# Performance work log

Hardware: AMD Instinct MI355X
Metric: run time of the kernel (lower is better)

## Reference

```python
import jax, jax.numpy as jnp
import numpy as np

BN_EPS = 1e-5


def _binary_activation(x):
    # forward value = sign(x); gradient flows through piecewise poly o3 (STE)
    s = jnp.sign(x)
    o1 = jnp.where(x < -1.0, -1.0, x * x + 2.0 * x)
    o2 = jnp.where(x < 0.0, o1, -x * x + 2.0 * x)
    o3 = jnp.where(x < 1.0, o2, 1.0)
    return jax.lax.stop_gradient(s - o3) + o3


def _binarize_weights(w):
    # sign_function: fwd 2*(w>0)-1, bwd identity (STE)
    sgn = 2.0 * (w > 0.0).astype(w.dtype) - 1.0
    wb = jax.lax.stop_gradient(sgn - w) + w
    # detached per-output-channel scale: mean |w| over (in, kh, kw)
    scale = jax.lax.stop_gradient(jnp.mean(jnp.abs(w), axis=(1, 2, 3), keepdims=True))
    return scale * wb


def setup_inputs() -> dict:
    key = jax.random.key(0)
    k1, k2, k3 = jax.random.split(key, 3)
    C = 64
    x = jax.random.normal(k1, (32, C, 112, 112), dtype=jnp.float32)
    w = jax.random.uniform(k2, (C, C, 3, 3), dtype=jnp.float32) * 0.001
    return {
        "x": x,
        "b0": jnp.zeros((1, C, 1, 1), jnp.float32),
        "w": w,
        "gamma": jnp.ones((C,), jnp.float32),
        "beta": jnp.zeros((C,), jnp.float32),
        "b1": jnp.zeros((1, C, 1, 1), jnp.float32),
        "alpha": jnp.full((C,), 0.25, jnp.float32),  # PReLU default init
        "b2": jnp.zeros((1, C, 1, 1), jnp.float32),
    }


def reference(x, b0, w, gamma, beta, b1, alpha, b2):
    residual = x
    out = x + b0                       # move0
    out = _binary_activation(out)      # binary activation
    bw = _binarize_weights(w)
    out = jax.lax.conv_general_dilated(
        out, bw, window_strides=(1, 1), padding=[(1, 1), (1, 1)],
        dimension_numbers=("NCHW", "OIHW", "NCHW"))
    # BatchNorm2d in training mode (batch stats, biased variance)
    mu = jnp.mean(out, axis=(0, 2, 3), keepdims=True)
    var = jnp.var(out, axis=(0, 2, 3), keepdims=True)
    g = gamma.reshape(1, -1, 1, 1)
    b = beta.reshape(1, -1, 1, 1)
    out = (out - mu) * jax.lax.rsqrt(var + BN_EPS) * g + b
    out = out + residual
    out = out + b1                     # move1
    a = alpha.reshape(1, -1, 1, 1)
    out = jnp.where(out > 0, out, a * out)  # PReLU
    out = out + b2                     # move2
    return out
```

## Files before the change

### kernel.cpp

```cpp
#include <hip/hip_runtime.h>
#include <stdint.h>

#define C 64
#define HH 112
#define WWD 112
#define HW (HH*WWD)
#define NB 32
#define MTOT (NB*HW)
#define PPR 56
#define PPI 6272
#define PACK_BLKS 1568
#define CONV_BLKS 25
#define OH 32

typedef unsigned long long u64t;

__global__ __launch_bounds__(256) void k_prep_pack(
        const float* __restrict__ x, const float* __restrict__ b0,
        const float* __restrict__ w,
        uint64_t* __restrict__ xp,
        uint64_t* __restrict__ wbits, float* __restrict__ wscale,
        int* __restrict__ corrP, int* __restrict__ ps, u64t* __restrict__ pq) {
    int bid = blockIdx.x;
    if (bid < PACK_BLKS) {
        int n = bid / 49;
        int pix = (bid % 49) * 256 + threadIdx.x;
        uint64_t p = 0;
        const float* xb = x + (size_t)n * C * HW + pix;
        #pragma unroll
        for (int c = 0; c < C; ++c) {
            float v = xb[(size_t)c * HW] + b0[c];
            p |= (uint64_t)(v > 0.f) << c;
        }
        xp[(size_t)n*HW + pix] = p;
    } else {
        int tid = threadIdx.x;
        int o = bid - PACK_BLKS;
        if (tid < 64) {
            int i = tid;
            const float* wp = w + ((size_t)o*C + i)*9;
            float s = 0.f;
            uint64_t b[9];
            #pragma unroll
            for (int k = 0; k < 9; ++k) {
                float v = wp[k];
                s += fabsf(v);
                b[k] = __ballot(v > 0.f);
            }
            #pragma unroll
            for (int off = 32; off > 0; off >>= 1) s += __shfl_down(s, off);
            if (i == 0) {
                wscale[o] = s * (1.0f/576.0f);
                int pq9[9];
                #pragma unroll
                for (int k = 0; k < 9; ++k) {
                    wbits[o*9+k] = b[k];
                    pq9[k] = __popcll(b[k]);
                }
                for (int rc = 0; rc < 3; ++rc)
                    for (int cc = 0; cc < 3; ++cc) {
                        int corr = 0;
                        for (int kr = 0; kr < 3; ++kr)
                            for (int kc = 0; kc < 3; ++kc) {
                                bool oob = (rc==0 && kr==0) || (rc==2 && kr==2) ||
                                           (cc==0 && kc==0) || (cc==2 && kc==2);
                                if (oob) corr += 64 - 2*pq9[kr*3+kc];
                            }
                        corrP[(rc*3+cc)*C + o] = 576 - corr;
                    }
            }
        } else if (bid == PACK_BLKS) {
            for (int i = tid - 64; i < C*8; i += 192) { ps[i] = 0; pq[i] = 0ull; }
        }
    }
}

__global__ __launch_bounds__(256) void k_convstats(
        const uint64_t* __restrict__ xp, const uint64_t* __restrict__ wbits,
        const int* __restrict__ corrP, int* __restrict__ ps, u64t* __restrict__ pq) {
    __shared__ uint64_t sq[OH*9];
    __shared__ int scor[9*OH];
    __shared__ int lsw[4][OH];
    __shared__ int lqw[4][OH];
    const int obase = blockIdx.z * OH;
    for (int i = threadIdx.x; i < OH*9; i += 256) sq[i] = wbits[obase*9 + i];
    for (int i = threadIdx.x; i < 9*OH; i += 256) {
        int r = i / OH, oo = i - r*OH;
        scor[i] = corrP[r*C + obase + oo];
    }
    __syncthreads();

    int n = blockIdx.y;
    int pr = blockIdx.x * 256 + threadIdx.x;
    int act = pr < PPI;
    int prc = act ? pr : (PPI - 1);
    int row = prc / PPR;
    int j   = prc - row * PPR;
    int c0  = 2 * j;
    const uint64_t* base = xp + (size_t)n * HW;
    uint64_t P[12];
    #pragma unroll
    for (int r = 0; r < 3; ++r) {
        int rr = row + r - 1;
        bool okr = (rr >= 0) & (rr < HH);
        #pragma unroll
        for (int c = 0; c < 4; ++c) {
            int cc = c0 + c - 1;
            bool ok = okr & (cc >= 0) & (cc < WWD);
            P[r*4+c] = ok ? base[(size_t)rr * WWD + cc] : 0ull;
        }
    }
    int rc   = (row == 0) ? 0 : ((row == HH-1) ? 2 : 1);
    int reg0 = (rc*3 + ((c0 == 0) ? 0 : 1)) * OH;
    int reg1 = (rc*3 + ((c0 == WWD-2) ? 2 : 1)) * OH;
    int wid = threadIdx.x >> 6, lane = threadIdx.x & 63;

    #pragma unroll 2
    for (int oo = 0; oo < OH; ++oo) {
        const uint64_t* q = &sq[oo*9];
        int a0 = 0, a1 = 0;
        #pragma unroll
        for (int r = 0; r < 3; ++r) {
            #pragma unroll
            for (int c = 0; c < 3; ++c) {
                uint64_t qk = q[r*3+c];
                a0 += __popcll(P[r*4+c]   ^ qk);
                a1 += __popcll(P[r*4+c+1] ^ qk);
            }
        }
        int v0 = scor[reg0 + oo] - 2*a0;
        int v1 = scor[reg1 + oo] - 2*a1;
        int s  = act ? (v0 + v1) : 0;
        int qq = act ? (v0*v0 + v1*v1) : 0;
        #pragma unroll
        for (int off = 1; off < 64; off <<= 1) {
            s  += __shfl_xor(s,  off);
            qq += __shfl_xor(qq, off);
        }
        if (lane == 0) { lsw[wid][oo] = s; lqw[wid][oo] = qq; }
    }
    __syncthreads();
    int t = threadIdx.x;
    int bkt = blockIdx.y & 7;
    if (t < OH) {
        int st = lsw[0][t] + lsw[1][t] + lsw[2][t] + lsw[3][t];
        atomicAdd(&ps[(obase + t)*8 + bkt], st);
    } else if (t < 2*OH) {
        int oo = t - OH;
        unsigned int qt = (unsigned)lqw[0][oo] + (unsigned)lqw[1][oo]
                        + (unsigned)lqw[2][oo] + (unsigned)lqw[3][oo];
        atomicAdd(&pq[(obase + oo)*8 + bkt], (u64t)qt);
    }
}

__global__ __launch_bounds__(256) void k_finish(
        const uint64_t* __restrict__ xp, const uint64_t* __restrict__ wbits,
        const int* __restrict__ corrP, const int* __restrict__ ps,
        const u64t* __restrict__ pq, const float* __restrict__ x,
        const float* __restrict__ wscale, const float* __restrict__ gamma,
        const float* __restrict__ beta, const float* __restrict__ b1,
        const float* __restrict__ alpha, const float* __restrict__ b2,
        float* __restrict__ out) {
    __shared__ uint64_t sq[OH*9];
    __shared__ int scor[9*OH];
    __shared__ float4 tab[OH];
    const int obase = blockIdx.z * OH;
    for (int i = threadIdx.x; i < OH*9; i += 256) sq[i] = wbits[obase*9 + i];
    for (int i = threadIdx.x; i < 9*OH; i += 256) {
        int r = i / OH, oo = i - r*OH;
        scor[i] = corrP[r*C + obase + oo];
    }
    if (threadIdx.x < OH) {
        int o = obase + threadIdx.x;
        int s = 0; u64t qv = 0;
        #pragma unroll
        for (int k = 0; k < 8; ++k) { s += ps[o*8+k]; qv += pq[o*8+k]; }
        const float inv = 1.0f / (float)MTOT;
        float sc   = wscale[o];
        float mean = (float)s * inv;
        float ek2  = (float)qv * inv;
        float mu   = sc * mean;
        float var  = sc*sc*ek2 - mu*mu;
        float g    = gamma[o] * rsqrtf(var + 1e-5f);
        tab[threadIdx.x] = make_float4(g*sc, beta[o] - g*mu + b1[o], alpha[o], b2[o]);
    }
    __syncthreads();

    int n = blockIdx.y;
    int pr = blockIdx.x * 256 + threadIdx.x;
    if (pr >= PPI) return;
    int row = pr / PPR;
    int j   = pr - row * PPR;
    int c0  = 2 * j;
    const uint64_t* base = xp + (size_t)n * HW;
    uint64_t P[12];
    #pragma unroll
    for (int r = 0; r < 3; ++r) {
        int rr = row + r - 1;
        bool okr = (rr >= 0) & (rr < HH);
        #pragma unroll
        for (int c = 0; c < 4; ++c) {
            int cc = c0 + c - 1;
            bool ok = okr & (cc >= 0) & (cc < WWD);
            P[r*4+c] = ok ? base[(size_t)rr * WWD + cc] : 0ull;
        }
    }
    int rc   = (row == 0) ? 0 : ((row == HH-1) ? 2 : 1);
    int reg0 = (rc*3 + ((c0 == 0) ? 0 : 1)) * OH;
    int reg1 = (rc*3 + ((c0 == WWD-2) ? 2 : 1)) * OH;

    int acc[OH];
    #pragma unroll
    for (int oo = 0; oo < OH; ++oo) {
        const uint64_t* q = &sq[oo*9];
        int a0 = 0, a1 = 0;
        #pragma unroll
        for (int r = 0; r < 3; ++r) {
            #pragma unroll
            for (int c = 0; c < 3; ++c) {
                uint64_t qk = q[r*3+c];
                a0 += __popcll(P[r*4+c]   ^ qk);
                a1 += __popcll(P[r*4+c+1] ^ qk);
            }
        }
        int v0 = scor[reg0 + oo] - 2*a0;
        int v1 = scor[reg1 + oo] - 2*a1;
        acc[oo] = (int)((uint32_t)(uint16_t)v0 | ((uint32_t)(uint16_t)v1 << 16));
    }

    const float2* x2 = (const float2*)x + ((size_t)n * C + obase) * (HW/2) + pr;
    float2*       o2 = (float2*)out     + ((size_t)n * C + obase) * (HW/2) + pr;
    #pragma unroll
    for (int oo = 0; oo < OH; ++oo) {
        int a = acc[oo];
        float v0 = (float)(int)(short)(a & 0xFFFF);
        float v1 = (float)(int)(short)((uint32_t)a >> 16);
        float4 t4 = tab[oo];
        float2 xv = x2[(size_t)oo * (HW/2)];
        float t0 = t4.x * v0 + t4.y + xv.x;
        float t1 = t4.x * v1 + t4.y + xv.y;
        t0 = t0 > 0.f ? t0 : t4.z * t0;
        t1 = t1 > 0.f ? t1 : t4.z * t1;
        o2[(size_t)oo * (HW/2)] = make_float2(t0 + t4.w, t1 + t4.w);
    }
}

extern "C" void kernel_launch(void* const* d_in, const int* in_sizes, int n_in,
                              void* d_out, int out_size, void* d_ws, size_t ws_size,
                              hipStream_t stream) {
    const float* x     = (const float*)d_in[0];
    const float* b0    = (const float*)d_in[1];
    const float* w     = (const float*)d_in[2];
    const float* gamma = (const float*)d_in[3];
    const float* beta  = (const float*)d_in[4];
    const float* b1    = (const float*)d_in[5];
    const float* alpha = (const float*)d_in[6];
    const float* b2    = (const float*)d_in[7];

    char* ws = (char*)d_ws;
    const size_t XPB = (size_t)NB * HW * sizeof(uint64_t);
    uint64_t* xp     = (uint64_t*)ws;
    uint64_t* wbits  = (uint64_t*)(ws + XPB);
    u64t*     pq     = (u64t*)(ws + XPB + 4608);
    float*    wscale = (float*)(ws + XPB + 4608 + 4096);
    int*      corrP  = (int*)(ws + XPB + 4608 + 4096 + 256);
    int*      ps     = (int*)(ws + XPB + 4608 + 4096 + 256 + 2304);

    hipLaunchKernelGGL(k_prep_pack, dim3(PACK_BLKS + 64), dim3(256), 0, stream,
                       x, b0, w, xp, wbits, wscale, corrP, ps, pq);
    hipLaunchKernelGGL(k_convstats, dim3(CONV_BLKS, NB, 2), dim3(256), 0, stream,
                       xp, wbits, corrP, ps, pq);
    hipLaunchKernelGGL(k_finish, dim3(CONV_BLKS, NB, 2), dim3(256), 0, stream,
                       xp, wbits, corrP, ps, pq, x, wscale, gamma, beta, b1, alpha, b2,
                       (float*)d_out);
}
```

Before: 126.3 us.

## Store packed conv results in output buffer instead of recomputing in finish

k_convstats now writes each pair of integer conv results, packed as two 16-bit values, into the output buffer as scratch. k_finish no longer recomputes the binary popcount convolution. Instead, one block per (n, channel) plane loads that plane's packed results into registers, synchronises, and overwrites the plane in place with the normalised, residual-added, PReLU output using float4 accesses. This removes the duplicate popcount compute but adds a full extra write and read of intermediate data through HBM.

```diff
diff --git a/kernel.cpp b/kernel.cpp
--- a/kernel.cpp
+++ b/kernel.cpp
@@ -12,6 +12,7 @@
 #define PACK_BLKS 1568
 #define CONV_BLKS 25
 #define OH 32
+#define FL4 3136
 
 typedef unsigned long long u64t;
 
@@ -77,7 +78,8 @@
 
 __global__ __launch_bounds__(256) void k_convstats(
         const uint64_t* __restrict__ xp, const uint64_t* __restrict__ wbits,
-        const int* __restrict__ corrP, int* __restrict__ ps, u64t* __restrict__ pq) {
+        const int* __restrict__ corrP, int* __restrict__ ps, u64t* __restrict__ pq,
+        uint32_t* __restrict__ cv) {
     __shared__ uint64_t sq[OH*9];
     __shared__ int scor[9*OH];
     __shared__ int lsw[4][OH];
@@ -115,6 +117,8 @@
     int reg1 = (rc*3 + ((c0 == WWD-2) ? 2 : 1)) * OH;
     int wid = threadIdx.x >> 6, lane = threadIdx.x & 63;
 
+    uint32_t* op = cv + ((size_t)n * C + obase) * HW + prc;
+
     #pragma unroll 2
     for (int oo = 0; oo < OH; ++oo) {
         const uint64_t* q = &sq[oo*9];
@@ -130,6 +134,8 @@
         }
         int v0 = scor[reg0 + oo] - 2*a0;
         int v1 = scor[reg1 + oo] - 2*a1;
+        if (act) op[(size_t)oo * HW] =
+            (uint32_t)(uint16_t)v0 | ((uint32_t)(uint16_t)v1 << 16);
         int s  = act ? (v0 + v1) : 0;
         int qq = act ? (v0*v0 + v1*v1) : 0;
         #pragma unroll
@@ -154,94 +160,55 @@
 }
 
 __global__ __launch_bounds__(256) void k_finish(
-        const uint64_t* __restrict__ xp, const uint64_t* __restrict__ wbits,
-        const int* __restrict__ corrP, const int* __restrict__ ps,
-        const u64t* __restrict__ pq, const float* __restrict__ x,
+        const uint32_t* __restrict__ cv, const float* __restrict__ x,
+        const int* __restrict__ ps, const u64t* __restrict__ pq,
         const float* __restrict__ wscale, const float* __restrict__ gamma,
         const float* __restrict__ beta, const float* __restrict__ b1,
         const float* __restrict__ alpha, const float* __restrict__ b2,
         float* __restrict__ out) {
-    __shared__ uint64_t sq[OH*9];
-    __shared__ int scor[9*OH];
-    __shared__ float4 tab[OH];
-    const int obase = blockIdx.z * OH;
-    for (int i = threadIdx.x; i < OH*9; i += 256) sq[i] = wbits[obase*9 + i];
-    for (int i = threadIdx.x; i < 9*OH; i += 256) {
-        int r = i / OH, oo = i - r*OH;
-        scor[i] = corrP[r*C + obase + oo];
-    }
-    if (threadIdx.x < OH) {
-        int o = obase + threadIdx.x;
-        int s = 0; u64t qv = 0;
-        #pragma unroll
-        for (int k = 0; k < 8; ++k) { s += ps[o*8+k]; qv += pq[o*8+k]; }
-        const float inv = 1.0f / (float)MTOT;
-        float sc   = wscale[o];
-        float mean = (float)s * inv;
-        float ek2  = (float)qv * inv;
-        float mu   = sc * mean;
-        float var  = sc*sc*ek2 - mu*mu;
-        float g    = gamma[o] * rsqrtf(var + 1e-5f);
-        tab[threadIdx.x] = make_float4(g*sc, beta[o] - g*mu + b1[o], alpha[o], b2[o]);
+    int o = blockIdx.x;
+    int n = blockIdx.y;
+    size_t plane = (size_t)n * C + o;
+
+    int s = 0; u64t qv = 0;
+    #pragma unroll
+    for (int k = 0; k < 8; ++k) { s += ps[o*8+k]; qv += pq[o*8+k]; }
+    const float inv = 1.0f / (float)MTOT;
+    float sc   = wscale[o];
+    float mean = (float)s * inv;
+    float ek2  = (float)qv * inv;
+    float mu   = sc * mean;
+    float var  = sc*sc*ek2 - mu*mu;
+    float g    = gamma[o] * rsqrtf(var + 1e-5f);
+    float A    = g * sc;
+    float B    = beta[o] - g*mu + b1[o];
+    float al   = alpha[o];
+    float bb2  = b2[o];
+
+    const uint2* cv2 = (const uint2*)cv + plane * (size_t)(HW/2);
+    uint2 rbuf[13];
+    #pragma unroll
+    for (int k = 0; k < 13; ++k) {
+        int i = threadIdx.x + k*256;
+        if (i < FL4) rbuf[k] = cv2[i];
     }
     __syncthreads();
 
-    int n = blockIdx.y;
-    int pr = blockIdx.x * 256 + threadIdx.x;
-    if (pr >= PPI) return;
-    int row = pr / PPR;
-    int j   = pr - row * PPR;
-    int c0  = 2 * j;
-    const uint64_t* base = xp + (size_t)n * HW;
-    uint64_t P[12];
-    #pragma unroll
-    for (int r = 0; r < 3; ++r) {
-        int rr = row + r - 1;
-        bool okr = (rr >= 0) & (rr < HH);
-        #pragma unroll
-        for (int c = 0; c < 4; ++c) {
-            int cc = c0 + c - 1;
-            bool ok = okr & (cc >= 0) & (cc < WWD);
-            P[r*4+c] = ok ? base[(size_t)rr * WWD + cc] : 0ull;
-        }
-    }
-    int rc   = (row == 0) ? 0 : ((row == HH-1) ? 2 : 1);
-    int reg0 = (rc*3 + ((c0 == 0) ? 0 : 1)) * OH;
-    int reg1 = (rc*3 + ((c0 == WWD-2) ? 2 : 1)) * OH;
-
-    int acc[OH];
-    #pragma unroll
-    for (int oo = 0; oo < OH; ++oo) {
-        const uint64_t* q = &sq[oo*9];
-        int a0 = 0, a1 = 0;
-        #pragma unroll
-        for (int r = 0; r < 3; ++r) {
-            #pragma unroll
-            for (int c = 0; c < 3; ++c) {
-                uint64_t qk = q[r*3+c];
-                a0 += __popcll(P[r*4+c]   ^ qk);
-                a1 += __popcll(P[r*4+c+1] ^ qk);
-            }
-        }
-        int v0 = scor[reg0 + oo] - 2*a0;
-        int v1 = scor[reg1 + oo] - 2*a1;
-        acc[oo] = (int)((uint32_t)(uint16_t)v0 | ((uint32_t)(uint16_t)v1 << 16));
-    }
-
-    const float2* x2 = (const float2*)x + ((size_t)n * C + obase) * (HW/2) + pr;
-    float2*       o2 = (float2*)out     + ((size_t)n * C + obase) * (HW/2) + pr;
-    #pragma unroll
-    for (int oo = 0; oo < OH; ++oo) {
-        int a = acc[oo];
-        float v0 = (float)(int)(short)(a & 0xFFFF);
-        float v1 = (float)(int)(short)((uint32_t)a >> 16);
-        float4 t4 = tab[oo];
-        float2 xv = x2[(size_t)oo * (HW/2)];
-        float t0 = t4.x * v0 + t4.y + xv.x;
-        float t1 = t4.x * v1 + t4.y + xv.y;
-        t0 = t0 > 0.f ? t0 : t4.z * t0;
-        t1 = t1 > 0.f ? t1 : t4.z * t1;
-        o2[(size_t)oo * (HW/2)] = make_float2(t0 + t4.w, t1 + t4.w);
+    const float4* x4 = (const float4*)x + plane * (size_t)FL4;
+    float4*       o4 = (float4*)out     + plane * (size_t)FL4;
+    #pragma unroll
+    for (int k = 0; k < 13; ++k) {
+        int i = threadIdx.x + k*256;
+        if (i < FL4) {
+            uint2 u = rbuf[k];
+            float4 xv = x4[i], r;
+            float t;
+            t = A * (float)(int)(short)(u.x & 0xFFFF) + B + xv.x; t = t > 0.f ? t : al*t; r.x = t + bb2;
+            t = A * (float)(int)(short)(u.x >> 16)    + B + xv.y; t = t > 0.f ? t : al*t; r.y = t + bb2;
+            t = A * (float)(int)(short)(u.y & 0xFFFF) + B + xv.z; t = t > 0.f ? t : al*t; r.z = t + bb2;
+            t = A * (float)(int)(short)(u.y >> 16)    + B + xv.w; t = t > 0.f ? t : al*t; r.w = t + bb2;
+            o4[i] = r;
+        }
     }
 }
 
@@ -266,11 +233,13 @@
     int*      corrP  = (int*)(ws + XPB + 4608 + 4096 + 256);
     int*      ps     = (int*)(ws + XPB + 4608 + 4096 + 256 + 2304);
 
+    uint32_t* cv = (uint32_t*)d_out;
+
     hipLaunchKernelGGL(k_prep_pack, dim3(PACK_BLKS + 64), dim3(256), 0, stream,
                        x, b0, w, xp, wbits, wscale, corrP, ps, pq);
     hipLaunchKernelGGL(k_convstats, dim3(CONV_BLKS, NB, 2), dim3(256), 0, stream,
-                       xp, wbits, corrP, ps, pq);
-    hipLaunchKernelGGL(k_finish, dim3(CONV_BLKS, NB, 2), dim3(256), 0, stream,
-                       xp, wbits, corrP, ps, pq, x, wscale, gamma, beta, b1, alpha, b2,
+                       xp, wbits, corrP, ps, pq, cv);
+    hipLaunchKernelGGL(k_finish, dim3(C, NB), dim3(256), 0, stream,
+                       cv, x, ps, pq, wscale, gamma, beta, b1, alpha, b2,
                        (float*)d_out);
 }
```

After: 120.9 us. 1.05x faster.
